# Performance work log

Measured on AMD Instinct MI355X. Metric: run time of the kernel, lower is better.

Reference implementation:

```python
import jax, jax.numpy as jnp
import numpy as np

N, E, D, H, L = 50000, 800000, 64, 1, 4
R_DIMS = [64, 32, 16, 16]
LN_EPS = 1e-6  # flax LayerNorm default


def _ln(x, s, b):
    m = jnp.mean(x, axis=-1, keepdims=True)
    v = jnp.mean(jnp.square(x - m), axis=-1, keepdims=True)
    return (x - m) / jnp.sqrt(v + LN_EPS) * s + b


def _jat_layer(x, edges, senders, receivers, mask, Wq, Wk, Wa, ln_s, ln_b, readout):
    # x: (N, H, D) node features
    n = x.shape[0]
    q = jnp.einsum('nab,abcd->ncd', x, Wq)   # (N, H, D) query projection
    k = jnp.einsum('nab,abcd->ncd', x, Wk)   # (N, H, D) key projection
    sq = q[senders]                           # (E, H, D) gather by sender
    rk = k[receivers]                         # (E, H, D) gather by receiver
    feat = jax.nn.swish(sq + rk)
    # per-head edge distance powers, as in the original code
    ep = jnp.reshape(jnp.stack([jnp.power(edges, i + 1) for i in range(H)], axis=0), (-1, H, 1))
    feat = jnp.concatenate([feat, ep], axis=-1)       # (E, H, D+1)
    logits = jnp.einsum('eab,abcd->ecd', feat, Wa)    # (E, H, 1)
    logits = logits + jnp.reshape(jnp.where(mask, 0.0, -jnp.inf), (-1, 1, 1))
    # segment softmax over receiver segments (stable)
    maxs = jax.ops.segment_max(logits, receivers, n)
    w = jnp.exp(logits - maxs[receivers])
    w = w / jax.ops.segment_sum(w, receivers, n)[receivers]
    new = jax.ops.segment_sum(sq * w, receivers, n)   # (N, H, D)
    new = jax.nn.swish(new) + x  # skip_proj is identity (same n_head, dim)
    if not readout:
        new = _ln(new, ln_s, ln_b)
    return new


def setup_inputs() -> dict:
    key = jax.random.key(0)
    ks = jax.random.split(key, 32)
    inp = {
        'nodes': jax.random.normal(ks[0], (N, D), jnp.float32),
        'edges': jax.random.uniform(ks[1], (E, 1), jnp.float32, 0.1, 5.0),
        'senders': jax.random.randint(ks[2], (E,), 0, N, jnp.int32),
        'receivers': jax.random.randint(ks[3], (E,), 0, N, jnp.int32),
        'mask': jnp.ones((E,), bool),
        'Wq': jax.random.normal(ks[4], (L, H, D, H, D), jnp.float32) / np.sqrt(D).astype(np.float32),
        'Wk': jax.random.normal(ks[5], (L, H, D, H, D), jnp.float32) / np.sqrt(D).astype(np.float32),
        'Wa': jax.random.normal(ks[6], (L, H, D + 1, H, 1), jnp.float32) / np.sqrt(D + 1).astype(np.float32),
        'ln_scale': jnp.ones((L - 1, D), jnp.float32),
        'ln_bias': jnp.zeros((L - 1, D), jnp.float32),
    }
    dims = [H * D] + R_DIMS
    for i in range(4):
        inp[f'Wr{i}'] = jax.random.normal(ks[7 + i], (dims[i], dims[i + 1]), jnp.float32) / np.sqrt(dims[i]).astype(np.float32)
        inp[f'rs{i}'] = jnp.ones((dims[i + 1],), jnp.float32)
        inp[f'rb{i}'] = jnp.zeros((dims[i + 1],), jnp.float32)
    inp['Wr4'] = jax.random.normal(ks[11], (R_DIMS[-1], 1), jnp.float32) / np.sqrt(R_DIMS[-1]).astype(np.float32)
    return inp


def reference(nodes, edges, senders, receivers, mask, Wq, Wk, Wa, ln_scale, ln_bias,
              Wr0, Wr1, Wr2, Wr3, Wr4, rs0, rs1, rs2, rs3, rb0, rb1, rb2, rb3):
    x = nodes[:, None, :]  # (N, 1, D): stack to head axis (first layer)
    for l in range(L):
        readout = (l == L - 1)
        ln_s = ln_scale[l] if not readout else None
        ln_b = ln_bias[l] if not readout else None
        x = _jat_layer(x, edges, senders, receivers, mask, Wq[l], Wk[l], Wa[l], ln_s, ln_b, readout)
    # pyramidal readout head [64:32:16:16:1]
    h = jnp.reshape(x, (x.shape[0], -1))
    for Wd, s, b in zip((Wr0, Wr1, Wr2, Wr3), (rs0, rs1, rs2, rs3), (rb0, rb1, rb2, rb3)):
        h = jax.nn.swish(_ln(h @ Wd, s, b))
    return jax.nn.swish(h @ Wr4)  # (N, 1) atomic contributions
```

## Files before the change

### kernel.cpp

```cpp
#include <hip/hip_runtime.h>

#define NN 50000
#define EE 800000

typedef unsigned short ushort_t;
typedef unsigned int uint_t;

__device__ __forceinline__ float swishf(float v) {
    return v / (1.f + __expf(-v));
}
__device__ __forceinline__ ushort_t f2bf(float f) {
    uint_t u = __float_as_uint(f);
    uint_t r = (u + 0x7fffu + ((u >> 16) & 1u)) >> 16;
    return (ushort_t)r;
}
__device__ __forceinline__ float bf2f(ushort_t h) {
    return __uint_as_float(((uint_t)h) << 16);
}

__global__ void __launch_bounds__(256) qk_kernel(
    const float* __restrict__ x, const float* __restrict__ Wq, const float* __restrict__ Wk,
    ushort_t* __restrict__ qbf, float* __restrict__ k)
{
    __shared__ float sWq[64 * 64];
    __shared__ float sWk[64 * 64];
    __shared__ float xrow[4][64];
    for (int i = threadIdx.x; i < 4096; i += 256) { sWq[i] = Wq[i]; sWk[i] = Wk[i]; }
    __syncthreads();
    const int lane = threadIdx.x & 63;
    const int winb = threadIdx.x >> 6;
    const int wave = (blockIdx.x * 256 + threadIdx.x) >> 6;
    const int nw = gridDim.x * 4;
    for (int row = wave; row < NN; row += nw) {
        xrow[winb][lane] = x[row * 64 + lane];
        float aq = 0.f, ak = 0.f;
#pragma unroll
        for (int b = 0; b < 64; ++b) {
            float xb = xrow[winb][b];
            aq = fmaf(xb, sWq[b * 64 + lane], aq);
            ak = fmaf(xb, sWk[b * 64 + lane], ak);
        }
        qbf[row * 64 + lane] = f2bf(aq);
        k[row * 64 + lane] = ak;
    }
}

__global__ void __launch_bounds__(256) hist_kernel(
    const int* __restrict__ receivers, int* __restrict__ counts)
{
    int e = blockIdx.x * 256 + threadIdx.x;
    int stride = gridDim.x * 256;
    for (; e < EE; e += stride) atomicAdd(counts + receivers[e], 1);
}

__global__ void __launch_bounds__(1024) scan_kernel(
    const int* __restrict__ counts, int* __restrict__ offsets)
{
    __shared__ int ts[1024];
    const int t = threadIdx.x;
    const int beg = t * 49;
    const int end = min(beg + 49, NN);
    int s = 0;
    for (int i = beg; i < end; ++i) s += counts[i];
    ts[t] = s;
    __syncthreads();
    for (int d = 1; d < 1024; d <<= 1) {
        int v = (t >= d) ? ts[t - d] : 0;
        __syncthreads();
        ts[t] += v;
        __syncthreads();
    }
    int ex = (t == 0) ? 0 : ts[t - 1];
    for (int i = beg; i < end; ++i) { offsets[i] = ex; ex += counts[i]; }
    if (t == 1023) offsets[NN] = ts[1023];
}

__global__ void __launch_bounds__(256) scatter_kernel(
    const int* __restrict__ receivers, const int* __restrict__ senders,
    const float* __restrict__ edges, const int* __restrict__ offsets,
    int* __restrict__ ctr, int* __restrict__ ssort, float* __restrict__ esort)
{
    int e = blockIdx.x * 256 + threadIdx.x;
    int stride = gridDim.x * 256;
    for (; e < EE; e += stride) {
        int r = receivers[e];
        int pos = atomicAdd(ctr + r, 1);
        int idx = offsets[r] + pos;
        ssort[idx] = senders[e];
        esort[idx] = edges[e];
    }
}

__global__ void __launch_bounds__(256) attn_kernel(
    const ushort_t* __restrict__ qbf, const float* __restrict__ k,
    const int* __restrict__ ssort, const float* __restrict__ esort,
    const int* __restrict__ offsets, const float* __restrict__ Wa,
    float* __restrict__ x, const float* __restrict__ ln_s,
    const float* __restrict__ ln_b, int do_ln)
{
    __shared__ ushort_t sQ[4][8][64];
    __shared__ float sWb[4][8];
    const int lane = threadIdx.x & 63;
    const int winb = threadIdx.x >> 6;
    const int wave = (blockIdx.x * 256 + threadIdx.x) >> 6;
    const int nw = gridDim.x * 4;
    const int c = lane & 7;
    const int e = lane >> 3;
    const int ofs = c * 8;
    float wac[8];
#pragma unroll
    for (int j = 0; j < 8; ++j) wac[j] = Wa[ofs + j];
    const float wa64 = Wa[64];
    const float lnsv = ln_s[lane], lnbv = ln_b[lane];

    for (int r = wave; r < NN; r += nw) {
        float kc[8];
        {
            const float4 k0 = *(const float4*)(k + (size_t)r * 64 + ofs);
            const float4 k1 = *(const float4*)(k + (size_t)r * 64 + ofs + 4);
            kc[0] = k0.x; kc[1] = k0.y; kc[2] = k0.z; kc[3] = k0.w;
            kc[4] = k1.x; kc[5] = k1.y; kc[6] = k1.z; kc[7] = k1.w;
        }
        const int beg = offsets[r], end = offsets[r + 1];
        float m = -3.0e38f, denp = 0.f, acc = 0.f;
        for (int i0 = beg; i0 < end; i0 += 8) {
            const int myi = i0 + e;
            const bool valid = myi < end;
            int s = 0; float ea = 0.f;
            if (valid) { s = ssort[myi]; ea = esort[myi]; }
            const uint4 qraw = *(const uint4*)(qbf + (size_t)s * 64 + ofs);
            float qv[8];
            qv[0] = __uint_as_float(qraw.x << 16);
            qv[1] = __uint_as_float(qraw.x & 0xFFFF0000u);
            qv[2] = __uint_as_float(qraw.y << 16);
            qv[3] = __uint_as_float(qraw.y & 0xFFFF0000u);
            qv[4] = __uint_as_float(qraw.z << 16);
            qv[5] = __uint_as_float(qraw.z & 0xFFFF0000u);
            qv[6] = __uint_as_float(qraw.w << 16);
            qv[7] = __uint_as_float(qraw.w & 0xFFFF0000u);
            float p = 0.f;
#pragma unroll
            for (int j = 0; j < 8; ++j) p = fmaf(swishf(qv[j] + kc[j]), wac[j], p);
            p += __shfl_xor(p, 1);
            p += __shfl_xor(p, 2);
            p += __shfl_xor(p, 4);
            const float logit = valid ? fmaf(ea, wa64, p) : -3.0e38f;
            float cm = logit;
            cm = fmaxf(cm, __shfl_xor(cm, 8));
            cm = fmaxf(cm, __shfl_xor(cm, 16));
            cm = fmaxf(cm, __shfl_xor(cm, 32));
            if (cm > m) {
                const float sc = __expf(m - cm);
                denp *= sc; acc *= sc; m = cm;
            }
            const float w = valid ? __expf(logit - m) : 0.f;
            denp += w;
            *(uint4*)(&sQ[winb][e][ofs]) = qraw;
            if (c == 0) sWb[winb][e] = w;
            __builtin_amdgcn_wave_barrier();
#pragma unroll
            for (int j = 0; j < 8; ++j)
                acc = fmaf(sWb[winb][j], bf2f(sQ[winb][j][lane]), acc);
            __builtin_amdgcn_wave_barrier();
        }
        float den = denp;
#pragma unroll
        for (int msk = 32; msk; msk >>= 1) den += __shfl_xor(den, msk);
        den *= 0.125f;
        float v = den > 0.f ? acc / den : 0.f;
        float nv = swishf(v) + x[(size_t)r * 64 + lane];
        if (do_ln) {
            float sum = nv;
#pragma unroll
            for (int msk = 32; msk; msk >>= 1) sum += __shfl_xor(sum, msk);
            const float mean = sum * (1.f / 64.f);
            const float d = nv - mean;
            float vs = d * d;
#pragma unroll
            for (int msk = 32; msk; msk >>= 1) vs += __shfl_xor(vs, msk);
            nv = d * rsqrtf(vs * (1.f / 64.f) + 1e-6f) * lnsv + lnbv;
        }
        x[(size_t)r * 64 + lane] = nv;
    }
}

template<int In, int Out>
__device__ __forceinline__ void dense(const float* __restrict__ h, float* __restrict__ y,
                                      const float* __restrict__ W)
{
#pragma unroll
    for (int j = 0; j < Out; ++j) y[j] = 0.f;
#pragma unroll
    for (int i = 0; i < In; ++i) {
        const float hi = h[i];
#pragma unroll
        for (int j = 0; j < Out; ++j) y[j] = fmaf(hi, W[i * Out + j], y[j]);
    }
}

template<int Dim>
__device__ __forceinline__ void ln_swish(float* __restrict__ v,
                                         const float* __restrict__ s,
                                         const float* __restrict__ b)
{
    float mean = 0.f;
#pragma unroll
    for (int d = 0; d < Dim; ++d) mean += v[d];
    mean *= (1.f / Dim);
    float var = 0.f;
#pragma unroll
    for (int d = 0; d < Dim; ++d) { const float t = v[d] - mean; var = fmaf(t, t, var); }
    const float inv = rsqrtf(var * (1.f / Dim) + 1e-6f);
#pragma unroll
    for (int d = 0; d < Dim; ++d) v[d] = swishf((v[d] - mean) * inv * s[d] + b[d]);
}

__global__ void __launch_bounds__(256) readout_kernel(
    const float* __restrict__ x,
    const float* __restrict__ W0, const float* __restrict__ rs0, const float* __restrict__ rb0,
    const float* __restrict__ W1, const float* __restrict__ rs1, const float* __restrict__ rb1,
    const float* __restrict__ W2, const float* __restrict__ rs2, const float* __restrict__ rb2,
    const float* __restrict__ W3, const float* __restrict__ rs3, const float* __restrict__ rb3,
    const float* __restrict__ W4, float* __restrict__ out)
{
    const int n = blockIdx.x * 256 + threadIdx.x;
    if (n >= NN) return;
    float h[64];
#pragma unroll
    for (int i = 0; i < 64; ++i) h[i] = x[(size_t)n * 64 + i];
    float y[64];
    dense<64, 64>(h, y, W0); ln_swish<64>(y, rs0, rb0);
    float z[32];
    dense<64, 32>(y, z, W1); ln_swish<32>(z, rs1, rb1);
    float u[16];
    dense<32, 16>(z, u, W2); ln_swish<16>(u, rs2, rb2);
    float v[16];
    dense<16, 16>(u, v, W3); ln_swish<16>(v, rs3, rb3);
    float p = 0.f;
#pragma unroll
    for (int i = 0; i < 16; ++i) p = fmaf(v[i], W4[i], p);
    out[n] = swishf(p);
}

extern "C" void kernel_launch(void* const* d_in, const int* in_sizes, int n_in,
                              void* d_out, int out_size, void* d_ws, size_t ws_size,
                              hipStream_t stream)
{
    const float* nodes     = (const float*)d_in[0];
    const float* edges     = (const float*)d_in[1];
    const int*   senders   = (const int*)d_in[2];
    const int*   receivers = (const int*)d_in[3];
    const float* Wq  = (const float*)d_in[5];
    const float* Wk  = (const float*)d_in[6];
    const float* Wa  = (const float*)d_in[7];
    const float* ln_s = (const float*)d_in[8];
    const float* ln_b = (const float*)d_in[9];
    const float* Wr0 = (const float*)d_in[10];
    const float* rs0 = (const float*)d_in[11];
    const float* rb0 = (const float*)d_in[12];
    const float* Wr1 = (const float*)d_in[13];
    const float* rs1 = (const float*)d_in[14];
    const float* rb1 = (const float*)d_in[15];
    const float* Wr2 = (const float*)d_in[16];
    const float* rs2 = (const float*)d_in[17];
    const float* rb2 = (const float*)d_in[18];
    const float* Wr3 = (const float*)d_in[19];
    const float* rs3 = (const float*)d_in[20];
    const float* rb3 = (const float*)d_in[21];
    const float* Wr4 = (const float*)d_in[22];
    float* out = (float*)d_out;

    float*    x       = (float*)d_ws;
    float*    k       = x + (size_t)NN * 64;
    ushort_t* qbf     = (ushort_t*)(k + (size_t)NN * 64);
    int*      counts  = (int*)(qbf + (size_t)NN * 64);
    int*      ctr     = counts + NN;
    int*      offsets = ctr + NN;
    int*      ssort   = offsets + NN + 1;
    float*    esort   = (float*)(ssort + EE);

    hipMemcpyAsync(x, nodes, (size_t)NN * 64 * sizeof(float), hipMemcpyDeviceToDevice, stream);

    hipMemsetAsync(counts, 0, 2 * NN * sizeof(int), stream);
    hist_kernel<<<3125, 256, 0, stream>>>(receivers, counts);
    scan_kernel<<<1, 1024, 0, stream>>>(counts, offsets);
    scatter_kernel<<<3125, 256, 0, stream>>>(receivers, senders, edges, offsets, ctr, ssort, esort);

    for (int l = 0; l < 4; ++l) {
        qk_kernel<<<1024, 256, 0, stream>>>(x, Wq + l * 4096, Wk + l * 4096, qbf, k);
        int lnidx = l < 3 ? l : 0;
        attn_kernel<<<3125, 256, 0, stream>>>(qbf, k, ssort, esort, offsets,
                                              Wa + l * 65, x,
                                              ln_s + lnidx * 64, ln_b + lnidx * 64,
                                              l < 3 ? 1 : 0);
    }
    readout_kernel<<<196, 256, 0, stream>>>(x, Wr0, rs0, rb0, Wr1, rs1, rb1,
                                            Wr2, rs2, rb2, Wr3, rs3, rb3, Wr4, out);
}
```

Measured before the change: 639.8 us.

## Register-resident QK weights, prefetch next edge chunk in attention, narrower readout blocks

```diff
diff --git a/kernel.cpp b/kernel.cpp
--- a/kernel.cpp
+++ b/kernel.cpp
@@ -22,26 +22,29 @@
     const float* __restrict__ x, const float* __restrict__ Wq, const float* __restrict__ Wk,
     ushort_t* __restrict__ qbf, float* __restrict__ k)
 {
-    __shared__ float sWq[64 * 64];
-    __shared__ float sWk[64 * 64];
-    __shared__ float xrow[4][64];
-    for (int i = threadIdx.x; i < 4096; i += 256) { sWq[i] = Wq[i]; sWk[i] = Wk[i]; }
-    __syncthreads();
     const int lane = threadIdx.x & 63;
-    const int winb = threadIdx.x >> 6;
     const int wave = (blockIdx.x * 256 + threadIdx.x) >> 6;
     const int nw = gridDim.x * 4;
+    float wq[64], wk[64];
+#pragma unroll
+    for (int b = 0; b < 64; ++b) {
+        wq[b] = Wq[b * 64 + lane];
+        wk[b] = Wk[b * 64 + lane];
+    }
     for (int row = wave; row < NN; row += nw) {
-        xrow[winb][lane] = x[row * 64 + lane];
-        float aq = 0.f, ak = 0.f;
-#pragma unroll
-        for (int b = 0; b < 64; ++b) {
-            float xb = xrow[winb][b];
-            aq = fmaf(xb, sWq[b * 64 + lane], aq);
-            ak = fmaf(xb, sWk[b * 64 + lane], ak);
+        const float* __restrict__ xr =
+            x + (size_t)((unsigned)__builtin_amdgcn_readfirstlane(row)) * 64;
+        float aq0 = 0.f, aq1 = 0.f, ak0 = 0.f, ak1 = 0.f;
+#pragma unroll
+        for (int b = 0; b < 64; b += 2) {
+            const float x0 = xr[b], x1 = xr[b + 1];
+            aq0 = fmaf(x0, wq[b], aq0);
+            ak0 = fmaf(x0, wk[b], ak0);
+            aq1 = fmaf(x1, wq[b + 1], aq1);
+            ak1 = fmaf(x1, wk[b + 1], ak1);
         }
-        qbf[row * 64 + lane] = f2bf(aq);
-        k[row * 64 + lane] = ak;
+        qbf[(size_t)row * 64 + lane] = f2bf(aq0 + aq1);
+        k[(size_t)row * 64 + lane] = ak0 + ak1;
     }
 }
 
@@ -121,14 +124,25 @@
             kc[0] = k0.x; kc[1] = k0.y; kc[2] = k0.z; kc[3] = k0.w;
             kc[4] = k1.x; kc[5] = k1.y; kc[6] = k1.z; kc[7] = k1.w;
         }
+        const float xv = x[(size_t)r * 64 + lane];
         const int beg = offsets[r], end = offsets[r + 1];
         float m = -3.0e38f, denp = 0.f, acc = 0.f;
-        for (int i0 = beg; i0 < end; i0 += 8) {
-            const int myi = i0 + e;
-            const bool valid = myi < end;
-            int s = 0; float ea = 0.f;
-            if (valid) { s = ssort[myi]; ea = esort[myi]; }
-            const uint4 qraw = *(const uint4*)(qbf + (size_t)s * 64 + ofs);
+
+        bool valid = (beg + e) < end;
+        int s = 0; float ea = 0.f;
+        if (valid) { s = ssort[beg + e]; ea = esort[beg + e]; }
+        uint4 qraw = *(const uint4*)(qbf + (size_t)s * 64 + ofs);
+
+        int i0 = beg;
+        while (i0 < end) {
+            const int ni0 = i0 + 8;
+            bool nvalid = false; int ns = 0; float nea = 0.f;
+            uint4 nqraw = qraw;
+            if (ni0 < end) {
+                nvalid = (ni0 + e) < end;
+                if (nvalid) { ns = ssort[ni0 + e]; nea = esort[ni0 + e]; }
+                nqraw = *(const uint4*)(qbf + (size_t)ns * 64 + ofs);
+            }
             float qv[8];
             qv[0] = __uint_as_float(qraw.x << 16);
             qv[1] = __uint_as_float(qraw.x & 0xFFFF0000u);
@@ -162,13 +176,15 @@
             for (int j = 0; j < 8; ++j)
                 acc = fmaf(sWb[winb][j], bf2f(sQ[winb][j][lane]), acc);
             __builtin_amdgcn_wave_barrier();
+            qraw = nqraw; ea = nea; valid = nvalid; i0 = ni0;
         }
+
         float den = denp;
 #pragma unroll
         for (int msk = 32; msk; msk >>= 1) den += __shfl_xor(den, msk);
         den *= 0.125f;
         float v = den > 0.f ? acc / den : 0.f;
-        float nv = swishf(v) + x[(size_t)r * 64 + lane];
+        float nv = swishf(v) + xv;
         if (do_ln) {
             float sum = nv;
 #pragma unroll
@@ -215,7 +231,7 @@
     for (int d = 0; d < Dim; ++d) v[d] = swishf((v[d] - mean) * inv * s[d] + b[d]);
 }
 
-__global__ void __launch_bounds__(256) readout_kernel(
+__global__ void __launch_bounds__(64, 1) readout_kernel(
     const float* __restrict__ x,
     const float* __restrict__ W0, const float* __restrict__ rs0, const float* __restrict__ rb0,
     const float* __restrict__ W1, const float* __restrict__ rs1, const float* __restrict__ rb1,
@@ -223,7 +239,7 @@
     const float* __restrict__ W3, const float* __restrict__ rs3, const float* __restrict__ rb3,
     const float* __restrict__ W4, float* __restrict__ out)
 {
-    const int n = blockIdx.x * 256 + threadIdx.x;
+    const int n = blockIdx.x * 64 + threadIdx.x;
     if (n >= NN) return;
     float h[64];
 #pragma unroll
@@ -287,13 +303,13 @@
     scatter_kernel<<<3125, 256, 0, stream>>>(receivers, senders, edges, offsets, ctr, ssort, esort);
 
     for (int l = 0; l < 4; ++l) {
-        qk_kernel<<<1024, 256, 0, stream>>>(x, Wq + l * 4096, Wk + l * 4096, qbf, k);
+        qk_kernel<<<512, 256, 0, stream>>>(x, Wq + l * 4096, Wk + l * 4096, qbf, k);
         int lnidx = l < 3 ? l : 0;
         attn_kernel<<<3125, 256, 0, stream>>>(qbf, k, ssort, esort, offsets,
                                               Wa + l * 65, x,
                                               ln_s + lnidx * 64, ln_b + lnidx * 64,
                                               l < 3 ? 1 : 0);
     }
-    readout_kernel<<<196, 256, 0, stream>>>(x, Wr0, rs0, rb0, Wr1, rs1, rb1,
-                                            Wr2, rs2, rb2, Wr3, rs3, rb3, Wr4, out);
-}
+    readout_kernel<<<784, 64, 0, stream>>>(x, Wr0, rs0, rb0, Wr1, rs1, rb1,
+                                           Wr2, rs2, rb2, Wr3, rs3, rb3, Wr4, out);
+}
```

Measured after the change: 648.0 us. Within noise of the previous version (+1.3%).
